# Kernel tuning notes

Measured on AMD Instinct MI355X. Metric: run time of the kernel, lower is better.

Reference implementation:

```python
import jax, jax.numpy as jnp
import numpy as np

B, N, C, D, H = 2, 1024, 64, 512, 16
HD = D // H
LENGTH_SCALE = 0.22
LN_EPS = 1e-5


def _ln(x, g, b):
    m = jnp.mean(x, axis=-1, keepdims=True)
    v = jnp.var(x, axis=-1, keepdims=True)
    return g * (x - m) * jax.lax.rsqrt(v + LN_EPS) + b


def _distance_affinity(positions, length_scale):
    # Gaussian affinity in [0,1]: exp(-||pi - pj||^2 / (2 ls^2))
    d2 = jnp.sum((positions[:, :, None, :] - positions[:, None, :, :]) ** 2, axis=-1)
    return jnp.exp(-d2 / (2.0 * length_scale * length_scale))


def setup_inputs() -> dict:
    key = jax.random.key(0)
    ks = jax.random.split(key, 24)
    p = lambda k, s: (jax.random.normal(k, s) * 0.02).astype(jnp.float32)
    hidden = jax.random.normal(ks[0], (B, N, D), jnp.float32)
    adjacency = (jax.random.uniform(ks[1], (B, N, N)) < 0.05).astype(jnp.float32)
    positions = jax.random.uniform(ks[2], (B, N, 2), jnp.float32)
    context_tokens = jax.random.normal(ks[3], (B, C, D), jnp.float32)
    edge_head_conditioning = (jax.random.normal(ks[4], (B, 4, N, N)) * 0.1).astype(jnp.float32)
    return {
        'hidden': hidden, 'adjacency': adjacency, 'positions': positions,
        'context_tokens': context_tokens, 'edge_head_conditioning': edge_head_conditioning,
        'Wq': p(ks[5], (D, D)), 'bq': jnp.zeros((D,), jnp.float32),
        'Wk': p(ks[6], (D, D)), 'bk': jnp.zeros((D,), jnp.float32),
        'Wv': p(ks[7], (D, D)), 'bv': jnp.zeros((D,), jnp.float32),
        'Wo': p(ks[8], (D, D)), 'bo': jnp.zeros((D,), jnp.float32),
        'ln1_g': jnp.ones((D,), jnp.float32), 'ln1_b': jnp.zeros((D,), jnp.float32),
        'ln2_g': jnp.ones((D,), jnp.float32), 'ln2_b': jnp.zeros((D,), jnp.float32),
        'W1': p(ks[9], (4 * D, D)), 'b1': jnp.zeros((4 * D,), jnp.float32),
        'W2': p(ks[10], (D, 4 * D)), 'b2': jnp.zeros((D,), jnp.float32),
    }


def _forward(hidden, adjacency, positions, context_tokens, edge_head_conditioning,
             Wq, bq, Wk, bk, Wv, bv, Wo, bo, ln1_g, ln1_b, ln2_g, ln2_b, W1, b1, W2, b2):
    b, n, d = hidden.shape
    cc = context_tokens.shape[1]
    hd = d // H
    n1 = _ln(hidden, ln1_g, ln1_b)
    nc = _ln(context_tokens, ln1_g, ln1_b)
    key_source = jnp.concatenate([n1, nc], axis=1)          # [b, m, d]
    m = n + cc
    q = (n1 @ Wq.T + bq).reshape(b, n, H, hd).transpose(0, 2, 1, 3)          # [b,h,n,hd]
    k = (key_source @ Wk.T + bk).reshape(b, m, H, hd).transpose(0, 2, 1, 3)  # [b,h,m,hd]
    v = (key_source @ Wv.T + bv).reshape(b, m, H, hd).transpose(0, 2, 1, 3)
    logits = jnp.einsum('bhnd,bhmd->bhnm', q, k) / jnp.sqrt(jnp.float32(hd))

    pad = jnp.zeros((b, n, cc), logits.dtype)
    dist_e = jnp.concatenate([_distance_affinity(positions, LENGTH_SCALE), pad], axis=-1)  # [b,n,m]
    adj_e = jnp.concatenate([adjacency, pad], axis=-1)                                      # [b,n,m]
    edge_e = jnp.concatenate([edge_head_conditioning,
                              jnp.zeros((b, 4, n, cc), logits.dtype)], axis=-1)             # [b,4,n,m]

    # heads 0:4 distance, 4:8 connectivity, 8:12 stress (edge cond), 12:16 free
    bias = jnp.concatenate([
        jnp.broadcast_to((2.0 * dist_e - 1.0)[:, None], (b, 4, n, m)),
        jnp.broadcast_to((2.0 * adj_e - 1.0)[:, None], (b, 4, n, m)),
        edge_e,
        jnp.zeros((b, 4, n, m), logits.dtype)], axis=1)
    scale = jnp.concatenate([
        jnp.broadcast_to((0.25 + 0.75 * dist_e)[:, None], (b, 4, n, m)),
        jnp.broadcast_to((0.25 + 0.75 * adj_e)[:, None], (b, 4, n, m)),
        jnp.ones((b, 8, n, m), logits.dtype)], axis=1)

    w = jax.nn.softmax(logits + bias, axis=-1) * scale
    w = w / jnp.maximum(jnp.sum(w, axis=-1, keepdims=True), 1e-6)
    att = jnp.einsum('bhnm,bhmd->bhnd', w, v).transpose(0, 2, 1, 3).reshape(b, n, d)
    hidden = hidden + att @ Wo.T + bo
    n2 = _ln(hidden, ln2_g, ln2_b)
    ff = jax.nn.gelu(n2 @ W1.T + b1, approximate=False) @ W2.T + b2
    return hidden + ff


def reference(hidden, adjacency, positions, context_tokens, edge_head_conditioning,
              Wq, bq, Wk, bk, Wv, bv, Wo, bo, ln1_g, ln1_b, ln2_g, ln2_b, W1, b1, W2, b2):
    return _forward(hidden, adjacency, positions, context_tokens, edge_head_conditioning,
                    Wq, bq, Wk, bk, Wv, bv, Wo, bo, ln1_g, ln1_b, ln2_g, ln2_b, W1, b1, W2, b2)
```

## Files before the change

### kernel.cpp

```cpp
#include <hip/hip_runtime.h>
#include <math.h>

typedef unsigned short u16;
typedef unsigned int u32;
typedef __attribute__((ext_vector_type(8))) short short8;
typedef __attribute__((ext_vector_type(8))) u16 ushort8_t;
typedef __attribute__((ext_vector_type(4))) u16 ushort4_t;
typedef __attribute__((ext_vector_type(4))) float floatx4;

#define DEV static __device__ __forceinline__

DEV u16 f2b(float f) {
    union { float f; u32 u; } v; v.f = f;
    u32 u = v.u;
    return (u16)((u + 0x7fffu + ((u >> 16) & 1u)) >> 16);
}
DEV float b2f(u16 h) {
    union { u32 u; float f; } v; v.u = ((u32)h) << 16;
    return v.f;
}
DEV float gelu_f(float x) {
    return 0.5f * x * (1.f + erff(x * 0.70710678118654752f));
}

__global__ __launch_bounds__(256) void cvt_ln(
    const float* __restrict__ wq, const float* __restrict__ wk,
    const float* __restrict__ wv, const float* __restrict__ wo,
    const float* __restrict__ w1, const float* __restrict__ w2,
    u16* __restrict__ oq, u16* __restrict__ ok, u16* __restrict__ ov,
    u16* __restrict__ oo, u16* __restrict__ o1, u16* __restrict__ o2,
    const float* __restrict__ hidden, const float* __restrict__ ctx,
    const float* __restrict__ g, const float* __restrict__ bta,
    u16* __restrict__ dst)
{
    if (blockIdx.x < 3072) {
        long i = ((long)blockIdx.x * 256 + threadIdx.x) * 4;
        const float* s; u16* d; long off;
        if (i < 1048576) {
            int seg = (int)(i >> 18);
            off = i & 262143;
            s = seg == 0 ? wq : seg == 1 ? wk : seg == 2 ? wv : wo;
            d = seg == 0 ? oq : seg == 1 ? ok : seg == 2 ? ov : oo;
        } else if (i < 2097152) {
            off = i - 1048576; s = w1; d = o1;
        } else {
            off = i - 2097152; s = w2; d = o2;
        }
        floatx4 v = *(const floatx4*)(s + off);
        ushort4_t r;
        r[0] = f2b(v[0]); r[1] = f2b(v[1]); r[2] = f2b(v[2]); r[3] = f2b(v[3]);
        *(ushort4_t*)(d + off) = r;
        return;
    }
    int wid = threadIdx.x >> 6, lane = threadIdx.x & 63;
    int row = (blockIdx.x - 3072) * 4 + wid;
    if (row >= 2176) return;
    int bi = row / 1088, loc = row % 1088;
    const float* src = (loc < 1024) ? hidden + ((long)(bi * 1024 + loc)) * 512
                                    : ctx + ((long)(bi * 64 + (loc - 1024))) * 512;
    const floatx4* p = (const floatx4*)(src + lane * 8);
    floatx4 a = p[0], b4 = p[1];
    float x[8];
    x[0] = a[0]; x[1] = a[1]; x[2] = a[2]; x[3] = a[3];
    x[4] = b4[0]; x[5] = b4[1]; x[6] = b4[2]; x[7] = b4[3];
    float s = 0.f, sq = 0.f;
#pragma unroll
    for (int j = 0; j < 8; j++) { s += x[j]; sq += x[j] * x[j]; }
#pragma unroll
    for (int m = 1; m < 64; m <<= 1) {
        s += __shfl_xor(s, m, 64);
        sq += __shfl_xor(sq, m, 64);
    }
    float mean = s * (1.f / 512.f);
    float var = sq * (1.f / 512.f) - mean * mean;
    float rstd = rsqrtf(var + 1e-5f);
    const floatx4* gp = (const floatx4*)(g + lane * 8);
    const floatx4* bp = (const floatx4*)(bta + lane * 8);
    floatx4 g0 = gp[0], g1 = gp[1], bb0 = bp[0], bb1 = bp[1];
    float gg[8], bbv[8];
    gg[0] = g0[0]; gg[1] = g0[1]; gg[2] = g0[2]; gg[3] = g0[3];
    gg[4] = g1[0]; gg[5] = g1[1]; gg[6] = g1[2]; gg[7] = g1[3];
    bbv[0] = bb0[0]; bbv[1] = bb0[1]; bbv[2] = bb0[2]; bbv[3] = bb0[3];
    bbv[4] = bb1[0]; bbv[5] = bb1[1]; bbv[6] = bb1[2]; bbv[7] = bb1[3];
    ushort8_t o;
#pragma unroll
    for (int j = 0; j < 8; j++) o[j] = f2b((x[j] - mean) * rstd * gg[j] + bbv[j]);
    *(ushort8_t*)(dst + (long)row * 512 + lane * 8) = o;
}

template<int ACT, int OMODE>
__global__ __launch_bounds__(256) void gemm_bt(
    const u16* __restrict__ A, const u16* __restrict__ Bw,
    const float* __restrict__ bias0, const float* __restrict__ bias1,
    const float* __restrict__ bias2,
    float* __restrict__ outf, u16* __restrict__ outb0,
    u16* __restrict__ outb1, u16* __restrict__ outb2,
    int M, int N, int K, int ksp)
{
    __shared__ u16 As[64 * 72];
    __shared__ u16 Bs[128 * 72];
    int tid = threadIdx.x;
    int wid = tid >> 6, lane = tid & 63;
    int l16 = lane & 15, lq = lane >> 4;
    int m0 = blockIdx.y * 64, n0 = blockIdx.x * 128;
    int wm = (wid >> 1) * 32, wn = (wid & 1) * 64;
    int srow = tid >> 3;
    int scol = (tid & 7) * 8;
    int kb0 = (OMODE >= 4) ? blockIdx.z * ksp : 0;
    int kend = (OMODE >= 4) ? kb0 + ksp : K;
    floatx4 acc[2][4] = {};
    const u16* Ap = A + (long)(m0 + srow) * K + scol;
    const u16* Bp = Bw + (long)(n0 + srow) * K + scol;
    ushort8_t pa[2], pb[4];
#pragma unroll
    for (int p = 0; p < 2; p++)
        pa[p] = *(const ushort8_t*)(Ap + (long)p * 32 * K + kb0);
#pragma unroll
    for (int p = 0; p < 4; p++)
        pb[p] = *(const ushort8_t*)(Bp + (long)p * 32 * K + kb0);
    for (int k0 = kb0; k0 < kend; k0 += 64) {
#pragma unroll
        for (int p = 0; p < 2; p++)
            *(ushort8_t*)(As + (p * 32 + srow) * 72 + scol) = pa[p];
#pragma unroll
        for (int p = 0; p < 4; p++)
            *(ushort8_t*)(Bs + (p * 32 + srow) * 72 + scol) = pb[p];
        __syncthreads();
        int k1 = k0 + 64;
        if (k1 < kend) {
#pragma unroll
            for (int p = 0; p < 2; p++)
                pa[p] = *(const ushort8_t*)(Ap + (long)p * 32 * K + k1);
#pragma unroll
            for (int p = 0; p < 4; p++)
                pb[p] = *(const ushort8_t*)(Bp + (long)p * 32 * K + k1);
        }
#pragma unroll
        for (int s = 0; s < 2; s++) {
            short8 af[2], bfr[4];
#pragma unroll
            for (int i = 0; i < 2; i++)
                af[i] = *(const short8*)(As + (wm + i * 16 + l16) * 72 + s * 32 + lq * 8);
#pragma unroll
            for (int j = 0; j < 4; j++)
                bfr[j] = *(const short8*)(Bs + (wn + j * 16 + l16) * 72 + s * 32 + lq * 8);
#pragma unroll
            for (int i = 0; i < 2; i++)
#pragma unroll
                for (int j = 0; j < 4; j++)
                    acc[i][j] = __builtin_amdgcn_mfma_f32_16x16x32_bf16(
                        af[i], bfr[j], acc[i][j], 0, 0, 0);
        }
        __syncthreads();
    }
    const float rs = 0.17677669529663687f;
#pragma unroll
    for (int i = 0; i < 2; i++) {
#pragma unroll
        for (int j = 0; j < 4; j++) {
            int gmb = m0 + wm + i * 16 + lq * 4;
            int gn = n0 + wn + j * 16 + l16;
#pragma unroll
            for (int r = 0; r < 4; r++) {
                int gm = gmb + r;
                float v = acc[i][j][r];
                if (OMODE == 1) {
                    v += bias0[gn];
                    if (ACT == 1) v = gelu_f(v);
                    outb0[(long)gm * N + gn] = f2b(v);
                } else if (OMODE == 3) {
                    if (gn < 512) {
                        outb0[(long)gm * 512 + gn] = f2b((v + bias0[gn]) * rs);
                    } else if (gn < 1024) {
                        outb1[(long)gm * 512 + gn - 512] = f2b(v + bias1[gn - 512]);
                    } else {
                        int bi = gm / 1088, tok = gm % 1088;
                        int col = gn - 1024;
                        outb2[((long)((bi * 16 + (col >> 5)) * 32 + (col & 31))) * 1088 + tok]
                            = f2b(v + bias2[col]);
                    }
                } else if (OMODE == 4) {
                    outf[((long)blockIdx.z * M + gm) * N + gn] = v;
                } else {
                    atomicAdd(outf + (long)gm * N + gn, v);
                }
            }
        }
    }
}

__global__ __launch_bounds__(256) void attn_kernel(
    const u16* __restrict__ qb, const u16* __restrict__ kb,
    const u16* __restrict__ vt, const float* __restrict__ adj,
    const float* __restrict__ pos, const float* __restrict__ ehc,
    float* __restrict__ o_part, float* __restrict__ l_part)
{
    __shared__ u16 P[4][1152];
    __shared__ u16 ub[4][1152];
    int b = blockIdx.z >> 2, split = blockIdx.z & 3;
    int h = blockIdx.y, grp = h >> 2;
    int qbase = blockIdx.x * 64;
    int tid = threadIdx.x, wid = tid >> 6, lane = tid & 63;
    int l16 = lane & 15, lq = lane >> 4;
    int kv_begin = (split == 0) ? 0 : 320 + (split - 1) * 256;
    int kv_end = (split == 3) ? 1088 : 320 + split * 256;
    const float inv2ls2 = 10.330578512396695f;
    float* pls = (float*)&ub[0][0];
    u16* bt = ub[wid];

    if (grp == 0) {
        for (int t = tid; t < 2048; t += 256) pls[t] = pos[b * 2048 + t];
        __syncthreads();
    }
    int rowbase = qbase + wid * 16;
    int qrow = rowbase + l16;
    short8 qa = *(const short8*)(qb + ((long)(b * 1088 + qrow)) * 512 + h * 32 + lq * 8);
    int irow[4];
#pragma unroll
    for (int r = 0; r < 4; r++) irow[r] = rowbase + lq * 4 + r;
    float ipx[4], ipy[4];
    if (grp == 0) {
#pragma unroll
        for (int r = 0; r < 4; r++) {
            ipx[r] = pls[irow[r] * 2];
            ipy[r] = pls[irow[r] * 2 + 1];
        }
    }

    bool stg = (grp == 1 || grp == 2);
    const float* src = (grp == 1)
        ? adj + ((long)(b * 1024 + rowbase)) * 1024
        : ehc + (((long)(b * 4 + (h - 8))) * 1024 + rowbase) * 1024;
    int row4 = lane >> 4, c16 = (lane & 15) * 4;
    floatx4 pre[4];

    float rsum[4] = {0.f, 0.f, 0.f, 0.f};
    floatx4 o[2] = {};
    floatx4 zacc = {0.f, 0.f, 0.f, 0.f};
    u16* Pw = P[wid];

    if (stg && kv_begin < 1024) {
#pragma unroll
        for (int p = 0; p < 4; p++)
            pre[p] = *(const floatx4*)(src + (long)(p * 4 + row4) * 1024 + kv_begin + c16);
#pragma unroll
        for (int p = 0; p < 4; p++) {
            ushort4_t w4;
#pragma unroll
            for (int e = 0; e < 4; e++) w4[e] = f2b(pre[p][e]);
            *(ushort4_t*)(bt + (p * 4 + row4) * 72 + c16) = w4;
        }
    }

    for (int kv = kv_begin; kv < kv_end; kv += 64) {
        floatx4 sfr[4];
#pragma unroll
        for (int jf = 0; jf < 4; jf++) {
            int tok = kv + jf * 16 + l16;
            short8 kf = *(const short8*)(kb + ((long)(b * 1088 + tok)) * 512 + h * 32 + lq * 8);
            sfr[jf] = __builtin_amdgcn_mfma_f32_16x16x32_bf16(qa, kf, zacc, 0, 0, 0);
        }
        int kvn = kv + 64;
        bool pf = stg && kvn < kv_end && kvn < 1024;
        if (pf) {
#pragma unroll
            for (int p = 0; p < 4; p++)
                pre[p] = *(const floatx4*)(src + (long)(p * 4 + row4) * 1024 + kvn + c16);
        }
#pragma unroll
        for (int jf = 0; jf < 4; jf++) {
            int j = kv + jf * 16 + l16;
            float px = 0.f, py = 0.f;
            if (grp == 0 && j < 1024) { px = pls[2 * j]; py = pls[2 * j + 1]; }
#pragma unroll
            for (int r = 0; r < 4; r++) {
                float bias, scale;
                if (grp == 0) {
                    if (j < 1024) {
                        float dx = ipx[r] - px, dy = ipy[r] - py;
                        float e = __expf(-(dx * dx + dy * dy) * inv2ls2);
                        bias = 2.f * e - 1.f; scale = 0.25f + 0.75f * e;
                    } else { bias = -1.f; scale = 0.25f; }
                } else if (grp == 1) {
                    if (j < 1024) {
                        float a = b2f(bt[(lq * 4 + r) * 72 + jf * 16 + l16]);
                        bias = 2.f * a - 1.f; scale = 0.25f + 0.75f * a;
                    } else { bias = -1.f; scale = 0.25f; }
                } else if (grp == 2) {
                    bias = (j < 1024) ? b2f(bt[(lq * 4 + r) * 72 + jf * 16 + l16]) : 0.f;
                    scale = 1.f;
                } else { bias = 0.f; scale = 1.f; }
                float sv = fminf(sfr[jf][r] + bias, 60.f);
                float p = __expf(sv) * scale;
                rsum[r] += p;
                Pw[(lq * 4 + r) * 72 + jf * 16 + l16] = f2b(p);
            }
        }
#pragma unroll
        for (int s = 0; s < 2; s++) {
            short8 pa = *(const short8*)(Pw + l16 * 72 + s * 32 + lq * 8);
#pragma unroll
            for (int nf = 0; nf < 2; nf++) {
                const u16* vrow = vt + ((long)((b * 16 + h) * 32 + nf * 16 + l16)) * 1088
                                  + kv + s * 32 + lq * 8;
                short8 vf = *(const short8*)vrow;
                o[nf] = __builtin_amdgcn_mfma_f32_16x16x32_bf16(pa, vf, o[nf], 0, 0, 0);
            }
        }
        if (pf) {
#pragma unroll
            for (int p = 0; p < 4; p++) {
                ushort4_t w4;
#pragma unroll
                for (int e = 0; e < 4; e++) w4[e] = f2b(pre[p][e]);
                *(ushort4_t*)(bt + (p * 4 + row4) * 72 + c16) = w4;
            }
        }
    }
#pragma unroll
    for (int r = 0; r < 4; r++) {
#pragma unroll
        for (int m = 1; m < 16; m <<= 1)
            rsum[r] += __shfl_xor(rsum[r], m, 64);
    }
    long pb = (((long)(split * 2 + b) * 16 + h) * 1024);
#pragma unroll
    for (int nf = 0; nf < 2; nf++)
#pragma unroll
        for (int r = 0; r < 4; r++)
            o_part[(pb + irow[r]) * 32 + nf * 16 + l16] = o[nf][r];
    if (l16 == 0) {
#pragma unroll
        for (int r = 0; r < 4; r++) l_part[pb + irow[r]] = rsum[r];
    }
}

__global__ __launch_bounds__(256) void attn_combine(
    const float* __restrict__ o_part, const float* __restrict__ l_part,
    u16* __restrict__ att)
{
    int idx = blockIdx.x * 256 + threadIdx.x;
    int c4 = idx & 7;
    int row = (idx >> 3) & 1023;
    int h = (idx >> 13) & 15;
    int b = (idx >> 17) & 1;
    long base = (((long)b * 16 + h) * 1024 + row) * 32 + c4 * 4;
    long lb0 = ((long)b * 16 + h) * 1024 + row;
    floatx4 a = {0.f, 0.f, 0.f, 0.f};
    float lsum = 0.f;
#pragma unroll
    for (int s = 0; s < 4; s++) {
        floatx4 p = *(const floatx4*)(o_part + (long)s * 1048576 + base);
#pragma unroll
        for (int e = 0; e < 4; e++) a[e] += p[e];
        lsum += l_part[(long)s * 32768 + lb0];
    }
    float inv = 1.f / lsum;
    ushort4_t w;
#pragma unroll
    for (int e = 0; e < 4; e++) w[e] = f2b(a[e] * inv);
    *(ushort4_t*)(att + ((long)b * 1024 + row) * 512 + h * 32 + c4 * 4) = w;
}

__global__ __launch_bounds__(256) void wo_ln2(
    const float* __restrict__ p0, const float* __restrict__ p1,
    const float* __restrict__ bo, const float* __restrict__ hidden,
    const float* __restrict__ g, const float* __restrict__ bta,
    const float* __restrict__ b2, float* __restrict__ out,
    u16* __restrict__ n2)
{
    int wid = threadIdx.x >> 6, lane = threadIdx.x & 63;
    int row = blockIdx.x * 4 + wid;
    long base = (long)row * 512 + lane * 8;
    float x[8];
#pragma unroll
    for (int hp = 0; hp < 2; hp++) {
        floatx4 a = *(const floatx4*)(hidden + base + hp * 4);
        floatx4 q0 = *(const floatx4*)(p0 + base + hp * 4);
        floatx4 q1 = *(const floatx4*)(p1 + base + hp * 4);
        floatx4 bb = *(const floatx4*)(bo + lane * 8 + hp * 4);
#pragma unroll
        for (int e = 0; e < 4; e++) x[hp * 4 + e] = a[e] + q0[e] + q1[e] + bb[e];
    }
    float s = 0.f, sq = 0.f;
#pragma unroll
    for (int j = 0; j < 8; j++) { s += x[j]; sq += x[j] * x[j]; }
#pragma unroll
    for (int m = 1; m < 64; m <<= 1) {
        s += __shfl_xor(s, m, 64);
        sq += __shfl_xor(sq, m, 64);
    }
    float mean = s * (1.f / 512.f);
    float var = sq * (1.f / 512.f) - mean * mean;
    float rstd = rsqrtf(var + 1e-5f);
#pragma unroll
    for (int hp = 0; hp < 2; hp++) {
        floatx4 bb2 = *(const floatx4*)(b2 + lane * 8 + hp * 4);
        floatx4 w;
#pragma unroll
        for (int e = 0; e < 4; e++) w[e] = x[hp * 4 + e] + bb2[e];
        *(floatx4*)(out + base + hp * 4) = w;
    }
    const floatx4* gp = (const floatx4*)(g + lane * 8);
    const floatx4* bp = (const floatx4*)(bta + lane * 8);
    floatx4 g0 = gp[0], g1 = gp[1], bb0 = bp[0], bb1 = bp[1];
    float gg[8], bbv[8];
    gg[0] = g0[0]; gg[1] = g0[1]; gg[2] = g0[2]; gg[3] = g0[3];
    gg[4] = g1[0]; gg[5] = g1[1]; gg[6] = g1[2]; gg[7] = g1[3];
    bbv[0] = bb0[0]; bbv[1] = bb0[1]; bbv[2] = bb0[2]; bbv[3] = bb0[3];
    bbv[4] = bb1[0]; bbv[5] = bb1[1]; bbv[6] = bb1[2]; bbv[7] = bb1[3];
    ushort8_t ov;
#pragma unroll
    for (int j = 0; j < 8; j++) ov[j] = f2b((x[j] - mean) * rstd * gg[j] + bbv[j]);
    *(ushort8_t*)(n2 + base) = ov;
}

extern "C" void kernel_launch(void* const* d_in, const int* in_sizes, int n_in,
                              void* d_out, int out_size, void* d_ws, size_t ws_size,
                              hipStream_t stream) {
    const float* hidden = (const float*)d_in[0];
    const float* adjacency = (const float*)d_in[1];
    const float* positions = (const float*)d_in[2];
    const float* context = (const float*)d_in[3];
    const float* ehc = (const float*)d_in[4];
    const float* Wq = (const float*)d_in[5];
    const float* bq = (const float*)d_in[6];
    const float* Wk = (const float*)d_in[7];
    const float* bk = (const float*)d_in[8];
    const float* Wv = (const float*)d_in[9];
    const float* bv = (const float*)d_in[10];
    const float* Wo = (const float*)d_in[11];
    const float* bo = (const float*)d_in[12];
    const float* ln1g = (const float*)d_in[13];
    const float* ln1b = (const float*)d_in[14];
    const float* ln2g = (const float*)d_in[15];
    const float* ln2b = (const float*)d_in[16];
    const float* W1 = (const float*)d_in[17];
    const float* b1 = (const float*)d_in[18];
    const float* W2 = (const float*)d_in[19];
    const float* b2 = (const float*)d_in[20];
    float* out = (float*)d_out;

    char* ws = (char*)d_ws;
    u16* wqkv_b = (u16*)(ws + 0);
    u16* wo_b   = (u16*)(ws + 1572864);
    u16* w1_b   = (u16*)(ws + 2097152);
    u16* w2_b   = (u16*)(ws + 4194304);
    u16* ks_b   = (u16*)(ws + 6291456);
    u16* q_b    = (u16*)(ws + 8519680);
    u16* k_b    = (u16*)(ws + 10747904);
    u16* vt_b   = (u16*)(ws + 12976128);
    u16* att_b  = (u16*)(ws + 15204352);
    u16* n2_b   = (u16*)(ws + 17301504);
    u16* g_b    = (u16*)(ws + 19398656);
    float* o_part = (float*)(ws + 27787264);
    float* l_part = (float*)(ws + 44564480);
    float* wo_p  = (float*)(ws + 45088768);

    cvt_ln<<<3616, 256, 0, stream>>>(Wq, Wk, Wv, Wo, W1, W2,
                                     wqkv_b, wqkv_b + 262144, wqkv_b + 524288,
                                     wo_b, w1_b, w2_b,
                                     hidden, context, ln1g, ln1b, ks_b);
    gemm_bt<0, 3><<<dim3(12, 34), 256, 0, stream>>>(
        ks_b, wqkv_b, bq, bk, bv, nullptr, q_b, k_b, vt_b, 2176, 1536, 512, 0);
    attn_kernel<<<dim3(16, 16, 8), 256, 0, stream>>>(
        q_b, k_b, vt_b, adjacency, positions, ehc, o_part, l_part);
    attn_combine<<<1024, 256, 0, stream>>>(o_part, l_part, att_b);
    gemm_bt<0, 4><<<dim3(4, 32, 2), 256, 0, stream>>>(
        att_b, wo_b, nullptr, nullptr, nullptr, wo_p, nullptr, nullptr, nullptr,
        2048, 512, 512, 256);
    wo_ln2<<<512, 256, 0, stream>>>(wo_p, wo_p + 1048576, bo, hidden,
                                    ln2g, ln2b, b2, out, n2_b);
    gemm_bt<1, 1><<<dim3(16, 32), 256, 0, stream>>>(
        n2_b, w1_b, b1, nullptr, nullptr, nullptr, g_b, nullptr, nullptr,
        2048, 2048, 512, 0);
    gemm_bt<0, 5><<<dim3(4, 32, 4), 256, 0, stream>>>(
        g_b, w2_b, nullptr, nullptr, nullptr, out, nullptr, nullptr, nullptr,
        2048, 512, 2048, 512);
}
```

Baseline: 226.5 us.

## Precompute distance affinity, enlarge GEMM tiles, halve attention KV splits

The distance-affinity matrix is now computed once per batch in bf16 inside the conversion kernel, so the attention kernel streams it instead of recomputing exp per head. The QKV and W1 GEMMs move to a new 128x128-tile kernel, and the split-K GEMMs become a separate kernel. Attention uses 2 KV splits instead of 4, which shrinks the combine step but launches half as many blocks. Packed bf16 conversion instructions and an unclamped exp are also introduced. The trade-off is an extra 4MB write and read for the affinity matrix, lower attention occupancy, and a possible overflow risk now that the exp clamp is gone.

```diff
diff --git a/kernel.cpp b/kernel.cpp
--- a/kernel.cpp
+++ b/kernel.cpp
@@ -6,6 +6,7 @@
 typedef __attribute__((ext_vector_type(8))) short short8;
 typedef __attribute__((ext_vector_type(8))) u16 ushort8_t;
 typedef __attribute__((ext_vector_type(4))) u16 ushort4_t;
+typedef __attribute__((ext_vector_type(2))) u32 uint2_t;
 typedef __attribute__((ext_vector_type(4))) float floatx4;
 
 #define DEV static __device__ __forceinline__
@@ -18,6 +19,11 @@
 DEV float b2f(u16 h) {
     union { u32 u; float f; } v; v.u = ((u32)h) << 16;
     return v.f;
+}
+DEV u32 cvt_pk(float lo, float hi) {
+    u32 r;
+    asm("v_cvt_pk_bf16_f32 %0, %1, %2" : "=v"(r) : "v"(lo), "v"(hi));
+    return r;
 }
 DEV float gelu_f(float x) {
     return 0.5f * x * (1.f + erff(x * 0.70710678118654752f));
@@ -31,7 +37,8 @@
     u16* __restrict__ oo, u16* __restrict__ o1, u16* __restrict__ o2,
     const float* __restrict__ hidden, const float* __restrict__ ctx,
     const float* __restrict__ g, const float* __restrict__ bta,
-    u16* __restrict__ dst)
+    u16* __restrict__ dst,
+    const float* __restrict__ pos, u16* __restrict__ ebt)
 {
     if (blockIdx.x < 3072) {
         long i = ((long)blockIdx.x * 256 + threadIdx.x) * 4;
@@ -52,6 +59,31 @@
         *(ushort4_t*)(d + off) = r;
         return;
     }
+    if (blockIdx.x >= 3616) {
+        const float inv2ls2 = 10.330578512396695f;
+        int t = blockIdx.x - 3616;
+        int b = t >> 10, i = t & 1023;
+        int j0 = threadIdx.x * 4;
+        float px = pos[((long)b * 1024 + i) * 2];
+        float py = pos[((long)b * 1024 + i) * 2 + 1];
+        floatx4 a = *(const floatx4*)(pos + (long)b * 2048 + j0 * 2);
+        floatx4 c = *(const floatx4*)(pos + (long)b * 2048 + j0 * 2 + 4);
+        float e[4];
+        {
+            float dx = px - a[0], dy = py - a[1];
+            e[0] = __expf(-(dx * dx + dy * dy) * inv2ls2);
+            dx = px - a[2]; dy = py - a[3];
+            e[1] = __expf(-(dx * dx + dy * dy) * inv2ls2);
+            dx = px - c[0]; dy = py - c[1];
+            e[2] = __expf(-(dx * dx + dy * dy) * inv2ls2);
+            dx = px - c[2]; dy = py - c[3];
+            e[3] = __expf(-(dx * dx + dy * dy) * inv2ls2);
+        }
+        ushort4_t r;
+        r[0] = f2b(e[0]); r[1] = f2b(e[1]); r[2] = f2b(e[2]); r[3] = f2b(e[3]);
+        *(ushort4_t*)(ebt + ((long)(b * 1024 + i)) * 1024 + j0) = r;
+        return;
+    }
     int wid = threadIdx.x >> 6, lane = threadIdx.x & 63;
     int row = (blockIdx.x - 3072) * 4 + wid;
     if (row >= 2176) return;
@@ -89,13 +121,100 @@
 }
 
 template<int ACT, int OMODE>
-__global__ __launch_bounds__(256) void gemm_bt(
+__global__ __launch_bounds__(256) void gemm_big(
     const u16* __restrict__ A, const u16* __restrict__ Bw,
     const float* __restrict__ bias0, const float* __restrict__ bias1,
     const float* __restrict__ bias2,
-    float* __restrict__ outf, u16* __restrict__ outb0,
-    u16* __restrict__ outb1, u16* __restrict__ outb2,
-    int M, int N, int K, int ksp)
+    u16* __restrict__ outb0, u16* __restrict__ outb1, u16* __restrict__ outb2,
+    int M, int N, int K)
+{
+    __shared__ u16 As[128 * 72];
+    __shared__ u16 Bs[128 * 72];
+    int tid = threadIdx.x;
+    int wid = tid >> 6, lane = tid & 63;
+    int l16 = lane & 15, lq = lane >> 4;
+    int m0 = blockIdx.y * 128, n0 = blockIdx.x * 128;
+    int wm = (wid >> 1) * 64, wn = (wid & 1) * 64;
+    int srow = tid >> 3;
+    int scol = (tid & 7) * 8;
+    floatx4 acc[4][4] = {};
+    const u16* Ap = A + (long)(m0 + srow) * K + scol;
+    const u16* Bp = Bw + (long)(n0 + srow) * K + scol;
+    ushort8_t pa[4], pb[4];
+#pragma unroll
+    for (int p = 0; p < 4; p++) {
+        pa[p] = *(const ushort8_t*)(Ap + (long)p * 32 * K);
+        pb[p] = *(const ushort8_t*)(Bp + (long)p * 32 * K);
+    }
+    for (int k0 = 0; k0 < K; k0 += 64) {
+#pragma unroll
+        for (int p = 0; p < 4; p++) {
+            *(ushort8_t*)(As + (p * 32 + srow) * 72 + scol) = pa[p];
+            *(ushort8_t*)(Bs + (p * 32 + srow) * 72 + scol) = pb[p];
+        }
+        __syncthreads();
+        int k1 = k0 + 64;
+        if (k1 < K) {
+#pragma unroll
+            for (int p = 0; p < 4; p++) {
+                pa[p] = *(const ushort8_t*)(Ap + (long)p * 32 * K + k1);
+                pb[p] = *(const ushort8_t*)(Bp + (long)p * 32 * K + k1);
+            }
+        }
+#pragma unroll
+        for (int s = 0; s < 2; s++) {
+            short8 af[4], bfr[4];
+#pragma unroll
+            for (int i = 0; i < 4; i++)
+                af[i] = *(const short8*)(As + (wm + i * 16 + l16) * 72 + s * 32 + lq * 8);
+#pragma unroll
+            for (int j = 0; j < 4; j++)
+                bfr[j] = *(const short8*)(Bs + (wn + j * 16 + l16) * 72 + s * 32 + lq * 8);
+#pragma unroll
+            for (int i = 0; i < 4; i++)
+#pragma unroll
+                for (int j = 0; j < 4; j++)
+                    acc[i][j] = __builtin_amdgcn_mfma_f32_16x16x32_bf16(
+                        af[i], bfr[j], acc[i][j], 0, 0, 0);
+        }
+        __syncthreads();
+    }
+    const float rs = 0.17677669529663687f;
+#pragma unroll
+    for (int i = 0; i < 4; i++) {
+#pragma unroll
+        for (int j = 0; j < 4; j++) {
+            int gmb = m0 + wm + i * 16 + lq * 4;
+            int gn = n0 + wn + j * 16 + l16;
+#pragma unroll
+            for (int r = 0; r < 4; r++) {
+                int gm = gmb + r;
+                float v = acc[i][j][r];
+                if (OMODE == 1) {
+                    v += bias0[gn];
+                    if (ACT == 1) v = gelu_f(v);
+                    outb0[(long)gm * N + gn] = f2b(v);
+                } else {
+                    if (gn < 512) {
+                        outb0[(long)gm * 512 + gn] = f2b((v + bias0[gn]) * rs);
+                    } else if (gn < 1024) {
+                        outb1[(long)gm * 512 + gn - 512] = f2b(v + bias1[gn - 512]);
+                    } else {
+                        int bi = gm / 1088, tok = gm % 1088;
+                        int col = gn - 1024;
+                        outb2[((long)((bi * 16 + (col >> 5)) * 32 + (col & 31))) * 1088 + tok]
+                            = f2b(v + bias2[col]);
+                    }
+                }
+            }
+        }
+    }
+}
+
+template<int OMODE>
+__global__ __launch_bounds__(256) void gemm_sk(
+    const u16* __restrict__ A, const u16* __restrict__ Bw,
+    float* __restrict__ outf, int M, int N, int K, int ksp)
 {
     __shared__ u16 As[64 * 72];
     __shared__ u16 Bs[128 * 72];
@@ -106,8 +225,8 @@
     int wm = (wid >> 1) * 32, wn = (wid & 1) * 64;
     int srow = tid >> 3;
     int scol = (tid & 7) * 8;
-    int kb0 = (OMODE >= 4) ? blockIdx.z * ksp : 0;
-    int kend = (OMODE >= 4) ? kb0 + ksp : K;
+    int kb0 = blockIdx.z * ksp;
+    int kend = kb0 + ksp;
     floatx4 acc[2][4] = {};
     const u16* Ap = A + (long)(m0 + srow) * K + scol;
     const u16* Bp = Bw + (long)(n0 + srow) * K + scol;
@@ -153,7 +272,6 @@
         }
         __syncthreads();
     }
-    const float rs = 0.17677669529663687f;
 #pragma unroll
     for (int i = 0; i < 2; i++) {
 #pragma unroll
@@ -164,22 +282,7 @@
             for (int r = 0; r < 4; r++) {
                 int gm = gmb + r;
                 float v = acc[i][j][r];
-                if (OMODE == 1) {
-                    v += bias0[gn];
-                    if (ACT == 1) v = gelu_f(v);
-                    outb0[(long)gm * N + gn] = f2b(v);
-                } else if (OMODE == 3) {
-                    if (gn < 512) {
-                        outb0[(long)gm * 512 + gn] = f2b((v + bias0[gn]) * rs);
-                    } else if (gn < 1024) {
-                        outb1[(long)gm * 512 + gn - 512] = f2b(v + bias1[gn - 512]);
-                    } else {
-                        int bi = gm / 1088, tok = gm % 1088;
-                        int col = gn - 1024;
-                        outb2[((long)((bi * 16 + (col >> 5)) * 32 + (col & 31))) * 1088 + tok]
-                            = f2b(v + bias2[col]);
-                    }
-                } else if (OMODE == 4) {
+                if (OMODE == 4) {
                     outf[((long)blockIdx.z * M + gm) * N + gn] = v;
                 } else {
                     atomicAdd(outf + (long)gm * N + gn, v);
@@ -192,63 +295,61 @@
 __global__ __launch_bounds__(256) void attn_kernel(
     const u16* __restrict__ qb, const u16* __restrict__ kb,
     const u16* __restrict__ vt, const float* __restrict__ adj,
-    const float* __restrict__ pos, const float* __restrict__ ehc,
+    const float* __restrict__ ehc, const u16* __restrict__ ebt,
     float* __restrict__ o_part, float* __restrict__ l_part)
 {
     __shared__ u16 P[4][1152];
     __shared__ u16 ub[4][1152];
-    int b = blockIdx.z >> 2, split = blockIdx.z & 3;
+    int b = blockIdx.z >> 1, split = blockIdx.z & 1;
     int h = blockIdx.y, grp = h >> 2;
     int qbase = blockIdx.x * 64;
     int tid = threadIdx.x, wid = tid >> 6, lane = tid & 63;
     int l16 = lane & 15, lq = lane >> 4;
-    int kv_begin = (split == 0) ? 0 : 320 + (split - 1) * 256;
-    int kv_end = (split == 3) ? 1088 : 320 + split * 256;
-    const float inv2ls2 = 10.330578512396695f;
-    float* pls = (float*)&ub[0][0];
+    int kv_begin = split ? 576 : 0;
+    int kv_end = split ? 1088 : 576;
     u16* bt = ub[wid];
-
-    if (grp == 0) {
-        for (int t = tid; t < 2048; t += 256) pls[t] = pos[b * 2048 + t];
-        __syncthreads();
-    }
+    u16* Pw = P[wid];
+
     int rowbase = qbase + wid * 16;
     int qrow = rowbase + l16;
     short8 qa = *(const short8*)(qb + ((long)(b * 1088 + qrow)) * 512 + h * 32 + lq * 8);
     int irow[4];
 #pragma unroll
     for (int r = 0; r < 4; r++) irow[r] = rowbase + lq * 4 + r;
-    float ipx[4], ipy[4];
-    if (grp == 0) {
-#pragma unroll
-        for (int r = 0; r < 4; r++) {
-            ipx[r] = pls[irow[r] * 2];
-            ipy[r] = pls[irow[r] * 2 + 1];
-        }
-    }
-
-    bool stg = (grp == 1 || grp == 2);
-    const float* src = (grp == 1)
+
+    bool stg = (grp <= 2);
+    const u16* srcb = ebt + ((long)(b * 1024 + rowbase)) * 1024;
+    const float* srcf = (grp == 1)
         ? adj + ((long)(b * 1024 + rowbase)) * 1024
         : ehc + (((long)(b * 4 + (h - 8))) * 1024 + rowbase) * 1024;
+    int r8 = lane >> 3, c8 = lane & 7;
     int row4 = lane >> 4, c16 = (lane & 15) * 4;
-    floatx4 pre[4];
+    ushort8_t preb[2];
+    floatx4 pref[4];
 
     float rsum[4] = {0.f, 0.f, 0.f, 0.f};
     floatx4 o[2] = {};
     floatx4 zacc = {0.f, 0.f, 0.f, 0.f};
-    u16* Pw = P[wid];
-
-    if (stg && kv_begin < 1024) {
-#pragma unroll
-        for (int p = 0; p < 4; p++)
-            pre[p] = *(const floatx4*)(src + (long)(p * 4 + row4) * 1024 + kv_begin + c16);
-#pragma unroll
-        for (int p = 0; p < 4; p++) {
-            ushort4_t w4;
-#pragma unroll
-            for (int e = 0; e < 4; e++) w4[e] = f2b(pre[p][e]);
-            *(ushort4_t*)(bt + (p * 4 + row4) * 72 + c16) = w4;
+
+    if (stg) {
+        if (grp == 0) {
+#pragma unroll
+            for (int p = 0; p < 2; p++)
+                preb[p] = *(const ushort8_t*)(srcb + (long)(p * 8 + r8) * 1024 + kv_begin + c8 * 8);
+#pragma unroll
+            for (int p = 0; p < 2; p++)
+                *(ushort8_t*)(bt + (p * 8 + r8) * 72 + c8 * 8) = preb[p];
+        } else {
+#pragma unroll
+            for (int p = 0; p < 4; p++)
+                pref[p] = *(const floatx4*)(srcf + (long)(p * 4 + row4) * 1024 + kv_begin + c16);
+#pragma unroll
+            for (int p = 0; p < 4; p++) {
+                uint2_t w;
+                w[0] = cvt_pk(pref[p][0], pref[p][1]);
+                w[1] = cvt_pk(pref[p][2], pref[p][3]);
+                *(uint2_t*)(bt + (p * 4 + row4) * 72 + c16) = w;
+            }
         }
     }
 
@@ -263,38 +364,37 @@
         int kvn = kv + 64;
         bool pf = stg && kvn < kv_end && kvn < 1024;
         if (pf) {
-#pragma unroll
-            for (int p = 0; p < 4; p++)
-                pre[p] = *(const floatx4*)(src + (long)(p * 4 + row4) * 1024 + kvn + c16);
-        }
-#pragma unroll
-        for (int jf = 0; jf < 4; jf++) {
-            int j = kv + jf * 16 + l16;
-            float px = 0.f, py = 0.f;
-            if (grp == 0 && j < 1024) { px = pls[2 * j]; py = pls[2 * j + 1]; }
-#pragma unroll
-            for (int r = 0; r < 4; r++) {
+            if (grp == 0) {
+#pragma unroll
+                for (int p = 0; p < 2; p++)
+                    preb[p] = *(const ushort8_t*)(srcb + (long)(p * 8 + r8) * 1024 + kvn + c8 * 8);
+            } else {
+#pragma unroll
+                for (int p = 0; p < 4; p++)
+                    pref[p] = *(const floatx4*)(srcf + (long)(p * 4 + row4) * 1024 + kvn + c16);
+            }
+        }
+#pragma unroll
+        for (int r = 0; r < 4; r++) {
+            float pv[4];
+#pragma unroll
+            for (int jf = 0; jf < 4; jf++) {
+                int j = kv + jf * 16 + l16;
+                float a = b2f(bt[(lq * 4 + r) * 72 + jf * 16 + l16]);
+                if (j >= 1024) a = 0.f;
                 float bias, scale;
-                if (grp == 0) {
-                    if (j < 1024) {
-                        float dx = ipx[r] - px, dy = ipy[r] - py;
-                        float e = __expf(-(dx * dx + dy * dy) * inv2ls2);
-                        bias = 2.f * e - 1.f; scale = 0.25f + 0.75f * e;
-                    } else { bias = -1.f; scale = 0.25f; }
-                } else if (grp == 1) {
-                    if (j < 1024) {
-                        float a = b2f(bt[(lq * 4 + r) * 72 + jf * 16 + l16]);
-                        bias = 2.f * a - 1.f; scale = 0.25f + 0.75f * a;
-                    } else { bias = -1.f; scale = 0.25f; }
-                } else if (grp == 2) {
-                    bias = (j < 1024) ? b2f(bt[(lq * 4 + r) * 72 + jf * 16 + l16]) : 0.f;
-                    scale = 1.f;
-                } else { bias = 0.f; scale = 1.f; }
-                float sv = fminf(sfr[jf][r] + bias, 60.f);
-                float p = __expf(sv) * scale;
+                if (grp <= 1) { bias = 2.f * a - 1.f; scale = 0.25f + 0.75f * a; }
+                else if (grp == 2) { bias = a; scale = 1.f; }
+                else { bias = 0.f; scale = 1.f; }
+                float p = __expf(sfr[jf][r] + bias) * scale;
                 rsum[r] += p;
-                Pw[(lq * 4 + r) * 72 + jf * 16 + l16] = f2b(p);
-            }
+                pv[jf] = p;
+            }
+            u32 pk0 = cvt_pk(pv[0], pv[1]);
+            u32 pk1 = cvt_pk(pv[2], pv[3]);
+            u16* prow = Pw + (lq * 4 + r) * 72 + l16;
+            prow[0] = (u16)pk0; prow[16] = (u16)(pk0 >> 16);
+            prow[32] = (u16)pk1; prow[48] = (u16)(pk1 >> 16);
         }
 #pragma unroll
         for (int s = 0; s < 2; s++) {
@@ -308,12 +408,18 @@
             }
         }
         if (pf) {
-#pragma unroll
-            for (int p = 0; p < 4; p++) {
-                ushort4_t w4;
-#pragma unroll
-                for (int e = 0; e < 4; e++) w4[e] = f2b(pre[p][e]);
-                *(ushort4_t*)(bt + (p * 4 + row4) * 72 + c16) = w4;
+            if (grp == 0) {
+#pragma unroll
+                for (int p = 0; p < 2; p++)
+                    *(ushort8_t*)(bt + (p * 8 + r8) * 72 + c8 * 8) = preb[p];
+            } else {
+#pragma unroll
+                for (int p = 0; p < 4; p++) {
+                    uint2_t w;
+                    w[0] = cvt_pk(pref[p][0], pref[p][1]);
+                    w[1] = cvt_pk(pref[p][2], pref[p][3]);
+                    *(uint2_t*)(bt + (p * 4 + row4) * 72 + c16) = w;
+                }
             }
         }
     }
@@ -346,19 +452,12 @@
     int b = (idx >> 17) & 1;
     long base = (((long)b * 16 + h) * 1024 + row) * 32 + c4 * 4;
     long lb0 = ((long)b * 16 + h) * 1024 + row;
-    floatx4 a = {0.f, 0.f, 0.f, 0.f};
-    float lsum = 0.f;
-#pragma unroll
-    for (int s = 0; s < 4; s++) {
-        floatx4 p = *(const floatx4*)(o_part + (long)s * 1048576 + base);
-#pragma unroll
-        for (int e = 0; e < 4; e++) a[e] += p[e];
-        lsum += l_part[(long)s * 32768 + lb0];
-    }
-    float inv = 1.f / lsum;
+    floatx4 a0 = *(const floatx4*)(o_part + base);
+    floatx4 a1 = *(const floatx4*)(o_part + 1048576 + base);
+    float inv = 1.f / (l_part[lb0] + l_part[32768 + lb0]);
     ushort4_t w;
 #pragma unroll
-    for (int e = 0; e < 4; e++) w[e] = f2b(a[e] * inv);
+    for (int e = 0; e < 4; e++) w[e] = f2b((a0[e] + a1[e]) * inv);
     *(ushort4_t*)(att + ((long)b * 1024 + row) * 512 + h * 32 + c4 * 4) = w;
 }
 
@@ -454,27 +553,26 @@
     u16* n2_b   = (u16*)(ws + 17301504);
     u16* g_b    = (u16*)(ws + 19398656);
     float* o_part = (float*)(ws + 27787264);
-    float* l_part = (float*)(ws + 44564480);
-    float* wo_p  = (float*)(ws + 45088768);
-
-    cvt_ln<<<3616, 256, 0, stream>>>(Wq, Wk, Wv, Wo, W1, W2,
+    float* l_part = (float*)(ws + 36175872);
+    float* wo_p  = (float*)(ws + 36438016);
+    u16* ebt_b   = (u16*)(ws + 44826624);
+
+    cvt_ln<<<5664, 256, 0, stream>>>(Wq, Wk, Wv, Wo, W1, W2,
                                      wqkv_b, wqkv_b + 262144, wqkv_b + 524288,
                                      wo_b, w1_b, w2_b,
-                                     hidden, context, ln1g, ln1b, ks_b);
-    gemm_bt<0, 3><<<dim3(12, 34), 256, 0, stream>>>(
-        ks_b, wqkv_b, bq, bk, bv, nullptr, q_b, k_b, vt_b, 2176, 1536, 512, 0);
-    attn_kernel<<<dim3(16, 16, 8), 256, 0, stream>>>(
-        q_b, k_b, vt_b, adjacency, positions, ehc, o_part, l_part);
+                                     hidden, context, ln1g, ln1b, ks_b,
+                                     positions, ebt_b);
+    gemm_big<0, 3><<<dim3(12, 17), 256, 0, stream>>>(
+        ks_b, wqkv_b, bq, bk, bv, q_b, k_b, vt_b, 2176, 1536, 512);
+    attn_kernel<<<dim3(16, 16, 4), 256, 0, stream>>>(
+        q_b, k_b, vt_b, adjacency, ehc, ebt_b, o_part, l_part);
     attn_combine<<<1024, 256, 0, stream>>>(o_part, l_part, att_b);
-    gemm_bt<0, 4><<<dim3(4, 32, 2), 256, 0, stream>>>(
-        att_b, wo_b, nullptr, nullptr, nullptr, wo_p, nullptr, nullptr, nullptr,
-        2048, 512, 512, 256);
+    gemm_sk<4><<<dim3(4, 32, 2), 256, 0, stream>>>(
+        att_b, wo_b, wo_p, 2048, 512, 512, 256);
     wo_ln2<<<512, 256, 0, stream>>>(wo_p, wo_p + 1048576, bo, hidden,
                                     ln2g, ln2b, b2, out, n2_b);
-    gemm_bt<1, 1><<<dim3(16, 32), 256, 0, stream>>>(
-        n2_b, w1_b, b1, nullptr, nullptr, nullptr, g_b, nullptr, nullptr,
-        2048, 2048, 512, 0);
-    gemm_bt<0, 5><<<dim3(4, 32, 4), 256, 0, stream>>>(
-        g_b, w2_b, nullptr, nullptr, nullptr, out, nullptr, nullptr, nullptr,
-        2048, 512, 2048, 512);
-}
+    gemm_big<1, 1><<<dim3(16, 16), 256, 0, stream>>>(
+        n2_b, w1_b, b1, nullptr, nullptr, g_b, nullptr, nullptr, 2048, 2048, 512);
+    gemm_sk<5><<<dim3(4, 32, 4), 256, 0, stream>>>(
+        g_b, w2_b, out, 2048, 512, 2048, 512);
+}
```

After: 238.4 us. 1.05x slower.
